# Performance work log

Measured on AMD Instinct MI355X. Metric: run time of the kernel, lower is better.

Reference implementation:

```python
import jax, jax.numpy as jnp
import numpy as np
import math

B, T, C, H, DFF = 4, 2048, 1024, 16, 4096
HD = C // H
EPS = 1e-5


def _layernorm(x, g, b):
    mu = jnp.mean(x, axis=-1, keepdims=True)
    var = jnp.var(x, axis=-1, keepdims=True)
    return (x - mu) * jax.lax.rsqrt(var + EPS) * g + b


def _new_gelu(x):
    # 0.5*x*(1+tanh(sqrt(2/pi)*(x+0.044715*x^3)))
    c = math.sqrt(2.0 / math.pi)
    return 0.5 * x * (1.0 + jnp.tanh(c * (x + 0.044715 * x ** 3)))


def setup_inputs() -> dict:
    key = jax.random.key(0)
    ks = jax.random.split(key, 12)
    s = lambda fan_in: 1.0 / math.sqrt(fan_in)
    return {
        "x": jax.random.normal(ks[0], (B, T, C), jnp.float32),
        "ln1_g": jnp.ones((C,), jnp.float32),
        "ln1_b": jnp.zeros((C,), jnp.float32),
        "w_qkv": jax.random.normal(ks[1], (C, 3 * C), jnp.float32) * s(C),
        "b_qkv": jnp.zeros((3 * C,), jnp.float32),
        "w_o": jax.random.normal(ks[2], (C, C), jnp.float32) * s(C),
        "b_o": jnp.zeros((C,), jnp.float32),
        "ln2_g": jnp.ones((C,), jnp.float32),
        "ln2_b": jnp.zeros((C,), jnp.float32),
        "w_fc": jax.random.normal(ks[3], (C, DFF), jnp.float32) * s(C),
        "b_fc": jnp.zeros((DFF,), jnp.float32),
        "w_proj": jax.random.normal(ks[4], (DFF, C), jnp.float32) * s(DFF),
        "b_proj": jnp.zeros((C,), jnp.float32),
    }


def reference(x, ln1_g, ln1_b, w_qkv, b_qkv, w_o, b_o, ln2_g, ln2_b, w_fc, b_fc, w_proj, b_proj):
    # --- attention sub-block ---
    h = _layernorm(x, ln1_g, ln1_b)
    qkv = h @ w_qkv + b_qkv                                  # (B,T,3C)
    q, k, v = jnp.split(qkv, 3, axis=-1)
    q = q.reshape(B, T, H, HD).transpose(0, 2, 1, 3)          # (B,H,T,hd)
    k = k.reshape(B, T, H, HD).transpose(0, 2, 1, 3)
    v = v.reshape(B, T, H, HD).transpose(0, 2, 1, 3)
    scores = jnp.einsum("bhqd,bhkd->bhqk", q, k) / math.sqrt(HD)
    causal = jnp.tril(jnp.ones((T, T), jnp.bool_))            # (T,T)
    scores = jnp.where(causal[None, None], scores, -jnp.inf)
    probs = jax.nn.softmax(scores, axis=-1)
    attn = jnp.einsum("bhqk,bhkd->bhqd", probs, v)
    attn = attn.transpose(0, 2, 1, 3).reshape(B, T, C)
    x = x + attn @ w_o + b_o
    # --- MLP sub-block ---
    h2 = _layernorm(x, ln2_g, ln2_b)
    x = x + _new_gelu(h2 @ w_fc + b_fc) @ w_proj + b_proj
    return x
```

## Files before the change

### kernel.cpp

```cpp
#include <hip/hip_runtime.h>
#include <hip/hip_bf16.h>

using bf16 = __hip_bfloat16;
typedef __attribute__((ext_vector_type(8))) short bf16x8;
typedef __attribute__((ext_vector_type(4))) float f32x4;
typedef __attribute__((ext_vector_type(16))) float f32x16;

#define LOG2E 1.4426950408889634f

__device__ inline short f2b(float f) {
  __hip_bfloat16 h = __float2bfloat16(f);
  return *reinterpret_cast<short*>(&h);
}
__device__ inline float b2f(short s) {
  unsigned int u = ((unsigned int)(unsigned short)s) << 16;
  float f;
  __builtin_memcpy(&f, &u, 4);
  return f;
}
__device__ inline unsigned pk2(float a, float b) {
  return (unsigned)(unsigned short)f2b(a) |
         ((unsigned)(unsigned short)f2b(b) << 16);
}

__global__ __launch_bounds__(256) void transpose_cast_kernel(
    const float* __restrict__ in, bf16* __restrict__ out, int K, int N) {
  __shared__ float tile[32][33];
  int tx = threadIdx.x & 31;
  int ty = threadIdx.x >> 5;
  int n0 = blockIdx.x * 32, k0 = blockIdx.y * 32;
#pragma unroll
  for (int i = 0; i < 4; i++)
    tile[ty + i * 8][tx] = in[(size_t)(k0 + ty + i * 8) * N + n0 + tx];
  __syncthreads();
#pragma unroll
  for (int i = 0; i < 4; i++)
    out[(size_t)(n0 + ty + i * 8) * K + k0 + tx] =
        __float2bfloat16(tile[tx][ty + i * 8]);
}

__global__ __launch_bounds__(256) void transpose_v_kernel(
    const bf16* __restrict__ qkv, bf16* __restrict__ vt) {
  __shared__ short tile[64][66];
  const int bh = blockIdx.y;
  const int b = bh >> 4, h = bh & 15;
  const int t0 = blockIdx.x * 64;
  const int tid = threadIdx.x;
  const int r = tid >> 3, c8 = (tid & 7) * 8;
#pragma unroll
  for (int p = 0; p < 2; p++) {
    int t = r + p * 32;
    bf16x8 v = *(const bf16x8*)&qkv[(size_t)(b * 2048 + t0 + t) * 3072 + 2048 +
                                    h * 64 + c8];
#pragma unroll
    for (int i = 0; i < 8; i++) tile[t][c8 + i] = v[i];
  }
  __syncthreads();
#pragma unroll
  for (int p = 0; p < 2; p++) {
    int d = r + p * 32;
    int tt = c8;
    bf16x8 o;
#pragma unroll
    for (int i = 0; i < 8; i++) o[i] = tile[tt + i][d];
    *(bf16x8*)&vt[(size_t)(bh * 64 + d) * 2048 + t0 + tt] = o;
  }
}

__global__ __launch_bounds__(256) void ln_kernel(
    const float* __restrict__ x, const float* __restrict__ g,
    const float* __restrict__ b, bf16* __restrict__ out) {
  int row = blockIdx.x;
  const float4 v = ((const float4*)(x + (size_t)row * 1024))[threadIdx.x];
  float s = v.x + v.y + v.z + v.w;
  float ss = v.x * v.x + v.y * v.y + v.z * v.z + v.w * v.w;
#pragma unroll
  for (int off = 1; off < 64; off <<= 1) {
    s += __shfl_xor(s, off);
    ss += __shfl_xor(ss, off);
  }
  __shared__ float red[2][4];
  int w = threadIdx.x >> 6, lane = threadIdx.x & 63;
  if (lane == 0) { red[0][w] = s; red[1][w] = ss; }
  __syncthreads();
  s = red[0][0] + red[0][1] + red[0][2] + red[0][3];
  ss = red[1][0] + red[1][1] + red[1][2] + red[1][3];
  float mu = s * (1.0f / 1024.0f);
  float var = ss * (1.0f / 1024.0f) - mu * mu;
  float rstd = rsqrtf(var + 1e-5f);
  const float4 gv = ((const float4*)g)[threadIdx.x];
  const float4 bv = ((const float4*)b)[threadIdx.x];
  short4 o4;
  o4.x = f2b((v.x - mu) * rstd * gv.x + bv.x);
  o4.y = f2b((v.y - mu) * rstd * gv.y + bv.y);
  o4.z = f2b((v.z - mu) * rstd * gv.z + bv.z);
  o4.w = f2b((v.w - mu) * rstd * gv.w + bv.w);
  ((short4*)out)[(size_t)row * 256 + threadIdx.x] = o4;
}

template <int EPI>
__global__ __launch_bounds__(256) void gemm_bt_kernel(
    const bf16* __restrict__ A, const bf16* __restrict__ Bt,
    const float* __restrict__ bias, const float* __restrict__ res,
    void* __restrict__ out, int M, int N, int K) {
  __shared__ short As[128 * 32];
  __shared__ short Bs[128 * 32];
  const int tid = threadIdx.x;
  const int w = tid >> 6, lane = tid & 63;
  const int wr = w >> 1, wc = w & 1;
  const int brow = blockIdx.y, bcol = blockIdx.x;

  f32x4 acc[4][4] = {};

  const int nk = K >> 5;
  for (int kt = 0; kt < nk; kt++) {
    __syncthreads();
#pragma unroll
    for (int j = 0; j < 2; j++) {
      int c = (j * 4 + w) * 64 + lane;
      int row = c >> 2, k8 = (c & 3) * 8;
      const bf16* ga = A + (size_t)(brow * 128 + row) * K + kt * 32 + k8;
      __builtin_amdgcn_global_load_lds(
          (const __attribute__((address_space(1))) unsigned int*)ga,
          (__attribute__((address_space(3))) unsigned int*)(As + (j * 4 + w) * 512),
          16, 0, 0);
      const bf16* gb = Bt + (size_t)(bcol * 128 + row) * K + kt * 32 + k8;
      __builtin_amdgcn_global_load_lds(
          (const __attribute__((address_space(1))) unsigned int*)gb,
          (__attribute__((address_space(3))) unsigned int*)(Bs + (j * 4 + w) * 512),
          16, 0, 0);
    }
    __syncthreads();
    bf16x8 af[4], bfr[4];
#pragma unroll
    for (int m = 0; m < 4; m++)
      af[m] = *(const bf16x8*)&As[(wr * 64 + m * 16 + (lane & 15)) * 32 +
                                  (lane >> 4) * 8];
#pragma unroll
    for (int n = 0; n < 4; n++)
      bfr[n] = *(const bf16x8*)&Bs[(wc * 64 + n * 16 + (lane & 15)) * 32 +
                                   (lane >> 4) * 8];
#pragma unroll
    for (int m = 0; m < 4; m++)
#pragma unroll
      for (int n = 0; n < 4; n++)
        acc[m][n] = __builtin_amdgcn_mfma_f32_16x16x32_bf16(af[m], bfr[n],
                                                            acc[m][n], 0, 0, 0);
  }

#pragma unroll
  for (int m = 0; m < 4; m++)
#pragma unroll
    for (int n = 0; n < 4; n++) {
      int gr0 = brow * 128 + wr * 64 + m * 16 + (lane >> 4) * 4;
      int gc = bcol * 128 + wc * 64 + n * 16 + (lane & 15);
      float bia = bias[gc];
#pragma unroll
      for (int j = 0; j < 4; j++) {
        float v = acc[m][n][j] + bia;
        size_t idx = (size_t)(gr0 + j) * N + gc;
        if constexpr (EPI == 0) {
          ((bf16*)out)[idx] = __float2bfloat16(v);
        } else if constexpr (EPI == 1) {
          ((float*)out)[idx] = v + res[idx];
        } else {
          float u = 0.7978845608028654f * (v + 0.044715f * v * v * v);
          float t = exp2f(u * (2.0f * LOG2E));
          float th = 1.0f - 2.0f / (t + 1.0f);
          ((bf16*)out)[idx] = __float2bfloat16(0.5f * v * (1.0f + th));
        }
      }
    }
}

__global__ __launch_bounds__(256) void attn_kernel(
    const bf16* __restrict__ qkv, const bf16* __restrict__ vt,
    bf16* __restrict__ attn) {
  const int bh = blockIdx.x;
  const int qt = blockIdx.y;
  const int b = bh >> 4, h = bh & 15;
  const int tid = threadIdx.x, w = tid >> 6, lane = tid & 63;
  const int col = lane & 31;
  const int hi = lane >> 5;

  __shared__ short Kl[64 * 64];
  __shared__ short Vl[64 * 64];

  const int qbase = qt * 128 + w * 32;
  const int qglob = qbase + col;
  const size_t qrow = (size_t)(b * 2048 + qglob);

  bf16x8 qf[4];
#pragma unroll
  for (int dks = 0; dks < 4; dks++) {
    bf16x8 raw =
        *(const bf16x8*)&qkv[qrow * 3072 + h * 64 + dks * 16 + hi * 8];
#pragma unroll
    for (int i = 0; i < 8; i++) qf[dks][i] = f2b(b2f(raw[i]) * 0.125f);
  }

  f32x16 ot[2] = {};
  float m = -1e30f, l = 0.0f;

  const int ktend = qt * 2 + 1;
  for (int kt = 0; kt <= ktend; kt++) {
    const int kv0 = kt * 64;
    __syncthreads();
#pragma unroll
    for (int j = 0; j < 2; j++) {
      int c = (j * 4 + w) * 64 + lane;
      int row = c >> 3;
      int sw8 = ((c & 7) ^ (row & 7)) * 8;
      const bf16* gk =
          qkv + (size_t)(b * 2048 + kv0 + row) * 3072 + 1024 + h * 64 + sw8;
      __builtin_amdgcn_global_load_lds(
          (const __attribute__((address_space(1))) unsigned int*)gk,
          (__attribute__((address_space(3))) unsigned int*)(Kl + (j * 4 + w) * 512),
          16, 0, 0);
      const bf16* gv = vt + (size_t)(bh * 64 + row) * 2048 + kv0 + sw8;
      __builtin_amdgcn_global_load_lds(
          (const __attribute__((address_space(1))) unsigned int*)gv,
          (__attribute__((address_space(3))) unsigned int*)(Vl + (j * 4 + w) * 512),
          16, 0, 0);
    }
    __syncthreads();

    if (kv0 <= qbase + 31) {
      f32x16 st[2] = {};
#pragma unroll
      for (int s = 0; s < 2; s++) {
        int kvrow = s * 32 + col;
        int swz = kvrow & 7;
#pragma unroll
        for (int dks = 0; dks < 4; dks++) {
          int ch = (dks * 2 + hi) ^ swz;
          bf16x8 kf = *(const bf16x8*)&Kl[kvrow * 64 + ch * 8];
          st[s] = __builtin_amdgcn_mfma_f32_32x32x16_bf16(kf, qf[dks], st[s],
                                                          0, 0, 0);
        }
      }
      if (kv0 + 63 > qbase) {
#pragma unroll
        for (int s = 0; s < 2; s++)
#pragma unroll
          for (int r = 0; r < 16; r++) {
            int kv = kv0 + s * 32 + (r & 3) + 8 * (r >> 2) + 4 * hi;
            if (kv > qglob) st[s][r] = -1e30f;
          }
      }
      float pmax = -1e30f;
#pragma unroll
      for (int s = 0; s < 2; s++)
#pragma unroll
        for (int r = 0; r < 16; r++) pmax = fmaxf(pmax, st[s][r]);
      pmax = fmaxf(pmax, __shfl_xor(pmax, 32));
      float mnew = fmaxf(m, pmax);
      float corr = exp2f((m - mnew) * LOG2E);
      m = mnew;
      float rs = 0.0f;
#pragma unroll
      for (int s = 0; s < 2; s++)
#pragma unroll
        for (int r = 0; r < 16; r++) {
          float pv = exp2f((st[s][r] - mnew) * LOG2E);
          st[s][r] = pv;
          rs += pv;
        }
      rs += __shfl_xor(rs, 32);
      l = l * corr + rs;
#pragma unroll
      for (int s = 0; s < 2; s++)
#pragma unroll
        for (int r = 0; r < 16; r++) ot[s][r] *= corr;

#pragma unroll
      for (int sub = 0; sub < 2; sub++) {
#pragma unroll
        for (int kl = 0; kl < 2; kl++) {
          unsigned A0 = pk2(st[sub][kl * 8 + 0], st[sub][kl * 8 + 1]);
          unsigned A1 = pk2(st[sub][kl * 8 + 2], st[sub][kl * 8 + 3]);
          unsigned B0 = pk2(st[sub][kl * 8 + 4], st[sub][kl * 8 + 5]);
          unsigned B1 = pk2(st[sub][kl * 8 + 6], st[sub][kl * 8 + 7]);
          unsigned sA0 = (unsigned)__shfl_xor((int)A0, 32);
          unsigned sA1 = (unsigned)__shfl_xor((int)A1, 32);
          unsigned sB0 = (unsigned)__shfl_xor((int)B0, 32);
          unsigned sB1 = (unsigned)__shfl_xor((int)B1, 32);
          union { unsigned u[4]; bf16x8 v; } pf;
          pf.u[0] = hi ? sB0 : A0;
          pf.u[1] = hi ? sB1 : A1;
          pf.u[2] = hi ? B0 : sA0;
          pf.u[3] = hi ? B1 : sA1;
          int ks = sub * 2 + kl;
#pragma unroll
          for (int ds = 0; ds < 2; ds++) {
            int drow = ds * 32 + col;
            int ch = (ks * 2 + hi) ^ (drow & 7);
            bf16x8 vf = *(const bf16x8*)&Vl[drow * 64 + ch * 8];
            ot[ds] = __builtin_amdgcn_mfma_f32_32x32x16_bf16(vf, pf.v, ot[ds],
                                                             0, 0, 0);
          }
        }
      }
    }
  }

  float rl = 1.0f / l;
#pragma unroll
  for (int ds = 0; ds < 2; ds++)
#pragma unroll
    for (int j = 0; j < 4; j++) {
      ushort4 o4;
      o4.x = (unsigned short)f2b(ot[ds][4 * j + 0] * rl);
      o4.y = (unsigned short)f2b(ot[ds][4 * j + 1] * rl);
      o4.z = (unsigned short)f2b(ot[ds][4 * j + 2] * rl);
      o4.w = (unsigned short)f2b(ot[ds][4 * j + 3] * rl);
      *(ushort4*)&attn[qrow * 1024 + h * 64 + 32 * ds + 8 * j + 4 * hi] = o4;
    }
}

extern "C" void kernel_launch(void* const* d_in, const int* in_sizes, int n_in,
                              void* d_out, int out_size, void* d_ws,
                              size_t ws_size, hipStream_t stream) {
  (void)in_sizes; (void)n_in; (void)out_size; (void)ws_size;
  const float* x      = (const float*)d_in[0];
  const float* ln1_g  = (const float*)d_in[1];
  const float* ln1_b  = (const float*)d_in[2];
  const float* w_qkv  = (const float*)d_in[3];
  const float* b_qkv  = (const float*)d_in[4];
  const float* w_o    = (const float*)d_in[5];
  const float* b_o    = (const float*)d_in[6];
  const float* ln2_g  = (const float*)d_in[7];
  const float* ln2_b  = (const float*)d_in[8];
  const float* w_fc   = (const float*)d_in[9];
  const float* b_fc   = (const float*)d_in[10];
  const float* w_proj = (const float*)d_in[11];
  const float* b_proj = (const float*)d_in[12];
  float* out = (float*)d_out;

  char* ws = (char*)d_ws;
  bf16* wt_qkv  = (bf16*)(ws + 0);
  bf16* wt_o    = (bf16*)(ws + 6291456);
  bf16* wt_fc   = (bf16*)(ws + 8388608);
  bf16* wt_proj = (bf16*)(ws + 16777216);
  float* x1     = (float*)(ws + 25165824);
  bf16* vtb     = (bf16*)(ws + 25165824);
  bf16* slotA   = (bf16*)(ws + 58720256);
  bf16* qkvb    = (bf16*)(ws + 75497472);
  bf16* gbuf    = (bf16*)(ws + 75497472);

  dim3 blk(256);
  transpose_cast_kernel<<<dim3(3072 / 32, 1024 / 32), blk, 0, stream>>>(
      w_qkv, wt_qkv, 1024, 3072);
  transpose_cast_kernel<<<dim3(1024 / 32, 1024 / 32), blk, 0, stream>>>(
      w_o, wt_o, 1024, 1024);
  transpose_cast_kernel<<<dim3(4096 / 32, 1024 / 32), blk, 0, stream>>>(
      w_fc, wt_fc, 1024, 4096);
  transpose_cast_kernel<<<dim3(1024 / 32, 4096 / 32), blk, 0, stream>>>(
      w_proj, wt_proj, 4096, 1024);

  ln_kernel<<<8192, blk, 0, stream>>>(x, ln1_g, ln1_b, slotA);
  gemm_bt_kernel<0><<<dim3(3072 / 128, 8192 / 128), blk, 0, stream>>>(
      slotA, wt_qkv, b_qkv, nullptr, qkvb, 8192, 3072, 1024);
  transpose_v_kernel<<<dim3(32, 64), blk, 0, stream>>>(qkvb, vtb);
  attn_kernel<<<dim3(64, 16), blk, 0, stream>>>(qkvb, vtb, slotA);
  gemm_bt_kernel<1><<<dim3(1024 / 128, 8192 / 128), blk, 0, stream>>>(
      slotA, wt_o, b_o, x, x1, 8192, 1024, 1024);
  ln_kernel<<<8192, blk, 0, stream>>>(x1, ln2_g, ln2_b, slotA);
  gemm_bt_kernel<2><<<dim3(4096 / 128, 8192 / 128), blk, 0, stream>>>(
      slotA, wt_fc, b_fc, nullptr, gbuf, 8192, 4096, 1024);
  gemm_bt_kernel<1><<<dim3(1024 / 128, 8192 / 128), blk, 0, stream>>>(
      gbuf, wt_proj, b_proj, x1, out, 8192, 1024, 4096);
}
```

Before: 471.3 us.

## Double-buffer attention K/V, add lazy softmax rescale, XCD-swizzle GEMM grid

The attention kernel now double-buffers K/V tiles in LDS, prefetching the next tile while computing the current one. It folds log2e into Q so the hardware v_exp_f32 can be used, and skips the running-max rescale unless the max grows by more than 8. It also processes query tiles in reverse order so the longest causal rows start first, and changes the LDS swizzle. The GEMMs use a 1D grid with a remapping intended to spread tiles across XCDs for better cache locality. Packed bf16 conversion instructions and a workspace re-layout are added; the lazy rescale and raw exp2 trade some numerical headroom for fewer instructions.

```diff
diff --git a/kernel.cpp b/kernel.cpp
--- a/kernel.cpp
+++ b/kernel.cpp
@@ -18,9 +18,15 @@
   __builtin_memcpy(&f, &u, 4);
   return f;
 }
-__device__ inline unsigned pk2(float a, float b) {
-  return (unsigned)(unsigned short)f2b(a) |
-         ((unsigned)(unsigned short)f2b(b) << 16);
+__device__ inline unsigned cvtpk(float a, float b) {
+  unsigned r;
+  asm("v_cvt_pk_bf16_f32 %0, %1, %2" : "=v"(r) : "v"(a), "v"(b));
+  return r;
+}
+__device__ inline float exp2_fast(float x) {
+  float r;
+  asm("v_exp_f32 %0, %1" : "=v"(r) : "v"(x));
+  return r;
 }
 
 __global__ __launch_bounds__(256) void transpose_cast_kernel(
@@ -90,16 +96,14 @@
   float rstd = rsqrtf(var + 1e-5f);
   const float4 gv = ((const float4*)g)[threadIdx.x];
   const float4 bv = ((const float4*)b)[threadIdx.x];
-  short4 o4;
-  o4.x = f2b((v.x - mu) * rstd * gv.x + bv.x);
-  o4.y = f2b((v.y - mu) * rstd * gv.y + bv.y);
-  o4.z = f2b((v.z - mu) * rstd * gv.z + bv.z);
-  o4.w = f2b((v.w - mu) * rstd * gv.w + bv.w);
-  ((short4*)out)[(size_t)row * 256 + threadIdx.x] = o4;
+  uint2 o2;
+  o2.x = cvtpk((v.x - mu) * rstd * gv.x + bv.x, (v.y - mu) * rstd * gv.y + bv.y);
+  o2.y = cvtpk((v.z - mu) * rstd * gv.z + bv.z, (v.w - mu) * rstd * gv.w + bv.w);
+  ((uint2*)out)[(size_t)row * 256 + threadIdx.x] = o2;
 }
 
 template <int EPI>
-__global__ __launch_bounds__(256) void gemm_bt_kernel(
+__global__ __launch_bounds__(256) void gemm128_kernel(
     const bf16* __restrict__ A, const bf16* __restrict__ Bt,
     const float* __restrict__ bias, const float* __restrict__ res,
     void* __restrict__ out, int M, int N, int K) {
@@ -108,7 +112,12 @@
   const int tid = threadIdx.x;
   const int w = tid >> 6, lane = tid & 63;
   const int wr = w >> 1, wc = w & 1;
-  const int brow = blockIdx.y, bcol = blockIdx.x;
+
+  const int nwg = gridDim.x;
+  const int gy = M >> 7;
+  const int flat = blockIdx.x;
+  const int sw = (flat & 7) * (nwg >> 3) + (flat >> 3);
+  const int bcol = sw / gy, brow = sw % gy;
 
   f32x4 acc[4][4] = {};
 
@@ -161,12 +170,12 @@
         size_t idx = (size_t)(gr0 + j) * N + gc;
         if constexpr (EPI == 0) {
           ((bf16*)out)[idx] = __float2bfloat16(v);
-        } else if constexpr (EPI == 1) {
+        } else if constexpr (EPI == 5) {
           ((float*)out)[idx] = v + res[idx];
         } else {
           float u = 0.7978845608028654f * (v + 0.044715f * v * v * v);
-          float t = exp2f(u * (2.0f * LOG2E));
-          float th = 1.0f - 2.0f / (t + 1.0f);
+          float t2 = exp2_fast(u * (2.0f * LOG2E));
+          float th = 1.0f - 2.0f / (t2 + 1.0f);
           ((bf16*)out)[idx] = __float2bfloat16(0.5f * v * (1.0f + th));
         }
       }
@@ -177,66 +186,82 @@
     const bf16* __restrict__ qkv, const bf16* __restrict__ vt,
     bf16* __restrict__ attn) {
   const int bh = blockIdx.x;
-  const int qt = blockIdx.y;
+  const int qt = 15 - blockIdx.y;
   const int b = bh >> 4, h = bh & 15;
   const int tid = threadIdx.x, w = tid >> 6, lane = tid & 63;
   const int col = lane & 31;
   const int hi = lane >> 5;
 
-  __shared__ short Kl[64 * 64];
-  __shared__ short Vl[64 * 64];
+  __shared__ short Kl[2][64 * 64];
+  __shared__ short Vl[2][64 * 64];
 
   const int qbase = qt * 128 + w * 32;
   const int qglob = qbase + col;
   const size_t qrow = (size_t)(b * 2048 + qglob);
 
-  bf16x8 qf[4];
+  union U8 { unsigned u[4]; bf16x8 v; };
+  U8 qf[4];
 #pragma unroll
   for (int dks = 0; dks < 4; dks++) {
     bf16x8 raw =
         *(const bf16x8*)&qkv[qrow * 3072 + h * 64 + dks * 16 + hi * 8];
 #pragma unroll
-    for (int i = 0; i < 8; i++) qf[dks][i] = f2b(b2f(raw[i]) * 0.125f);
-  }
-
-  f32x16 ot[2] = {};
-  float m = -1e30f, l = 0.0f;
-
-  const int ktend = qt * 2 + 1;
-  for (int kt = 0; kt <= ktend; kt++) {
-    const int kv0 = kt * 64;
-    __syncthreads();
+    for (int p = 0; p < 4; p++)
+      qf[dks].u[p] = cvtpk(b2f(raw[2 * p]) * (0.125f * LOG2E),
+                           b2f(raw[2 * p + 1]) * (0.125f * LOG2E));
+  }
+
+  auto stage = [&](int kt, int buf) {
+    const int kv0s = kt * 64;
 #pragma unroll
     for (int j = 0; j < 2; j++) {
       int c = (j * 4 + w) * 64 + lane;
       int row = c >> 3;
-      int sw8 = ((c & 7) ^ (row & 7)) * 8;
+      int sw8 = ((c & 7) ^ ((row >> 1) & 7)) * 8;
       const bf16* gk =
-          qkv + (size_t)(b * 2048 + kv0 + row) * 3072 + 1024 + h * 64 + sw8;
+          qkv + (size_t)(b * 2048 + kv0s + row) * 3072 + 1024 + h * 64 + sw8;
       __builtin_amdgcn_global_load_lds(
           (const __attribute__((address_space(1))) unsigned int*)gk,
-          (__attribute__((address_space(3))) unsigned int*)(Kl + (j * 4 + w) * 512),
+          (__attribute__((address_space(3))) unsigned int*)(
+              &Kl[buf][(j * 4 + w) * 512]),
           16, 0, 0);
-      const bf16* gv = vt + (size_t)(bh * 64 + row) * 2048 + kv0 + sw8;
+      const bf16* gv = vt + (size_t)(bh * 64 + row) * 2048 + kv0s + sw8;
       __builtin_amdgcn_global_load_lds(
           (const __attribute__((address_space(1))) unsigned int*)gv,
-          (__attribute__((address_space(3))) unsigned int*)(Vl + (j * 4 + w) * 512),
+          (__attribute__((address_space(3))) unsigned int*)(
+              &Vl[buf][(j * 4 + w) * 512]),
           16, 0, 0);
     }
-    __syncthreads();
+  };
+
+  f32x16 ot[2] = {};
+  float m = -1e30f, l = 0.0f;
+
+  const int ktend = qt * 2 + 1;
+  stage(0, 0);
+  for (int kt = 0; kt <= ktend; kt++) {
+    const int kv0 = kt * 64;
+    const int cur = kt & 1;
+    if (kt < ktend) {
+      stage(kt + 1, cur ^ 1);
+      asm volatile("s_waitcnt vmcnt(4)" ::: "memory");
+    } else {
+      asm volatile("s_waitcnt vmcnt(0)" ::: "memory");
+    }
+    __builtin_amdgcn_s_barrier();
 
     if (kv0 <= qbase + 31) {
       f32x16 st[2] = {};
 #pragma unroll
       for (int s = 0; s < 2; s++) {
         int kvrow = s * 32 + col;
-        int swz = kvrow & 7;
+        int swz = (kvrow >> 1) & 7;
 #pragma unroll
         for (int dks = 0; dks < 4; dks++) {
           int ch = (dks * 2 + hi) ^ swz;
-          bf16x8 kf = *(const bf16x8*)&Kl[kvrow * 64 + ch * 8];
-          st[s] = __builtin_amdgcn_mfma_f32_32x32x16_bf16(kf, qf[dks], st[s],
-                                                          0, 0, 0);
+          bf16x8 kf = *(const bf16x8*)&Kl[cur][kvrow * 64 + ch * 8];
+          st[s] = __builtin_amdgcn_mfma_f32_32x32x16_bf16(kf, qf[dks].v,
+                                                          st[s], 0, 0, 0);
         }
       }
       if (kv0 + 63 > qbase) {
@@ -248,44 +273,50 @@
             if (kv > qglob) st[s][r] = -1e30f;
           }
       }
-      float pmax = -1e30f;
+      float vm[16];
+#pragma unroll
+      for (int i = 0; i < 16; i++) vm[i] = fmaxf(st[0][i], st[1][i]);
+#pragma unroll
+      for (int w2 = 8; w2 >= 1; w2 >>= 1)
+#pragma unroll
+        for (int i = 0; i < w2; i++) vm[i] = fmaxf(vm[i], vm[i + w2]);
+      float pmax = fmaxf(vm[0], __shfl_xor(vm[0], 32));
+      if (!__all(pmax - m <= 8.0f)) {
+        float mnew = fmaxf(m, pmax);
+        float corr = exp2_fast(m - mnew);
+        m = mnew;
+        l *= corr;
+#pragma unroll
+        for (int s = 0; s < 2; s++)
+#pragma unroll
+          for (int r = 0; r < 16; r++) ot[s][r] *= corr;
+      }
 #pragma unroll
       for (int s = 0; s < 2; s++)
 #pragma unroll
-        for (int r = 0; r < 16; r++) pmax = fmaxf(pmax, st[s][r]);
-      pmax = fmaxf(pmax, __shfl_xor(pmax, 32));
-      float mnew = fmaxf(m, pmax);
-      float corr = exp2f((m - mnew) * LOG2E);
-      m = mnew;
-      float rs = 0.0f;
-#pragma unroll
-      for (int s = 0; s < 2; s++)
-#pragma unroll
-        for (int r = 0; r < 16; r++) {
-          float pv = exp2f((st[s][r] - mnew) * LOG2E);
-          st[s][r] = pv;
-          rs += pv;
-        }
-      rs += __shfl_xor(rs, 32);
-      l = l * corr + rs;
-#pragma unroll
-      for (int s = 0; s < 2; s++)
-#pragma unroll
-        for (int r = 0; r < 16; r++) ot[s][r] *= corr;
+        for (int r = 0; r < 16; r++) st[s][r] = exp2_fast(st[s][r] - m);
+      float vs[16];
+#pragma unroll
+      for (int i = 0; i < 16; i++) vs[i] = st[0][i] + st[1][i];
+#pragma unroll
+      for (int w2 = 8; w2 >= 1; w2 >>= 1)
+#pragma unroll
+        for (int i = 0; i < w2; i++) vs[i] += vs[i + w2];
+      l += vs[0] + __shfl_xor(vs[0], 32);
 
 #pragma unroll
       for (int sub = 0; sub < 2; sub++) {
 #pragma unroll
         for (int kl = 0; kl < 2; kl++) {
-          unsigned A0 = pk2(st[sub][kl * 8 + 0], st[sub][kl * 8 + 1]);
-          unsigned A1 = pk2(st[sub][kl * 8 + 2], st[sub][kl * 8 + 3]);
-          unsigned B0 = pk2(st[sub][kl * 8 + 4], st[sub][kl * 8 + 5]);
-          unsigned B1 = pk2(st[sub][kl * 8 + 6], st[sub][kl * 8 + 7]);
+          unsigned A0 = cvtpk(st[sub][kl * 8 + 0], st[sub][kl * 8 + 1]);
+          unsigned A1 = cvtpk(st[sub][kl * 8 + 2], st[sub][kl * 8 + 3]);
+          unsigned B0 = cvtpk(st[sub][kl * 8 + 4], st[sub][kl * 8 + 5]);
+          unsigned B1 = cvtpk(st[sub][kl * 8 + 6], st[sub][kl * 8 + 7]);
           unsigned sA0 = (unsigned)__shfl_xor((int)A0, 32);
           unsigned sA1 = (unsigned)__shfl_xor((int)A1, 32);
           unsigned sB0 = (unsigned)__shfl_xor((int)B0, 32);
           unsigned sB1 = (unsigned)__shfl_xor((int)B1, 32);
-          union { unsigned u[4]; bf16x8 v; } pf;
+          U8 pf;
           pf.u[0] = hi ? sB0 : A0;
           pf.u[1] = hi ? sB1 : A1;
           pf.u[2] = hi ? B0 : sA0;
@@ -294,14 +325,15 @@
 #pragma unroll
           for (int ds = 0; ds < 2; ds++) {
             int drow = ds * 32 + col;
-            int ch = (ks * 2 + hi) ^ (drow & 7);
-            bf16x8 vf = *(const bf16x8*)&Vl[drow * 64 + ch * 8];
+            int ch = (ks * 2 + hi) ^ ((drow >> 1) & 7);
+            bf16x8 vf = *(const bf16x8*)&Vl[cur][drow * 64 + ch * 8];
             ot[ds] = __builtin_amdgcn_mfma_f32_32x32x16_bf16(vf, pf.v, ot[ds],
                                                              0, 0, 0);
           }
         }
       }
     }
+    __builtin_amdgcn_s_barrier();
   }
 
   float rl = 1.0f / l;
@@ -309,12 +341,10 @@
   for (int ds = 0; ds < 2; ds++)
 #pragma unroll
     for (int j = 0; j < 4; j++) {
-      ushort4 o4;
-      o4.x = (unsigned short)f2b(ot[ds][4 * j + 0] * rl);
-      o4.y = (unsigned short)f2b(ot[ds][4 * j + 1] * rl);
-      o4.z = (unsigned short)f2b(ot[ds][4 * j + 2] * rl);
-      o4.w = (unsigned short)f2b(ot[ds][4 * j + 3] * rl);
-      *(ushort4*)&attn[qrow * 1024 + h * 64 + 32 * ds + 8 * j + 4 * hi] = o4;
+      uint2 o2;
+      o2.x = cvtpk(ot[ds][4 * j + 0] * rl, ot[ds][4 * j + 1] * rl);
+      o2.y = cvtpk(ot[ds][4 * j + 2] * rl, ot[ds][4 * j + 3] * rl);
+      *(uint2*)&attn[qrow * 1024 + h * 64 + 32 * ds + 8 * j + 4 * hi] = o2;
     }
 }
 
@@ -338,15 +368,16 @@
   float* out = (float*)d_out;
 
   char* ws = (char*)d_ws;
-  bf16* wt_qkv  = (bf16*)(ws + 0);
-  bf16* wt_o    = (bf16*)(ws + 6291456);
-  bf16* wt_fc   = (bf16*)(ws + 8388608);
-  bf16* wt_proj = (bf16*)(ws + 16777216);
-  float* x1     = (float*)(ws + 25165824);
-  bf16* vtb     = (bf16*)(ws + 25165824);
-  bf16* slotA   = (bf16*)(ws + 58720256);
-  bf16* qkvb    = (bf16*)(ws + 75497472);
-  bf16* gbuf    = (bf16*)(ws + 75497472);
+  const size_t MB = 1048576;
+  float* x1     = (float*)(ws + 0);
+  bf16* slotA   = (bf16*)(ws + 32 * MB);
+  bf16* wt_qkv  = (bf16*)(ws + 48 * MB);
+  bf16* wt_o    = (bf16*)(ws + 54 * MB);
+  bf16* wt_fc   = (bf16*)(ws + 56 * MB);
+  bf16* wt_proj = (bf16*)(ws + 64 * MB);
+  bf16* qkvb    = (bf16*)(ws + 72 * MB);
+  bf16* vtb     = (bf16*)(ws + 120 * MB);
+  bf16* gbuf    = (bf16*)(ws + 72 * MB);
 
   dim3 blk(256);
   transpose_cast_kernel<<<dim3(3072 / 32, 1024 / 32), blk, 0, stream>>>(
@@ -359,15 +390,15 @@
       w_proj, wt_proj, 4096, 1024);
 
   ln_kernel<<<8192, blk, 0, stream>>>(x, ln1_g, ln1_b, slotA);
-  gemm_bt_kernel<0><<<dim3(3072 / 128, 8192 / 128), blk, 0, stream>>>(
+  gemm128_kernel<0><<<dim3(1536), blk, 0, stream>>>(
       slotA, wt_qkv, b_qkv, nullptr, qkvb, 8192, 3072, 1024);
   transpose_v_kernel<<<dim3(32, 64), blk, 0, stream>>>(qkvb, vtb);
   attn_kernel<<<dim3(64, 16), blk, 0, stream>>>(qkvb, vtb, slotA);
-  gemm_bt_kernel<1><<<dim3(1024 / 128, 8192 / 128), blk, 0, stream>>>(
+  gemm128_kernel<5><<<dim3(512), blk, 0, stream>>>(
       slotA, wt_o, b_o, x, x1, 8192, 1024, 1024);
   ln_kernel<<<8192, blk, 0, stream>>>(x1, ln2_g, ln2_b, slotA);
-  gemm_bt_kernel<2><<<dim3(4096 / 128, 8192 / 128), blk, 0, stream>>>(
+  gemm128_kernel<2><<<dim3(2048), blk, 0, stream>>>(
       slotA, wt_fc, b_fc, nullptr, gbuf, 8192, 4096, 1024);
-  gemm_bt_kernel<1><<<dim3(1024 / 128, 8192 / 128), blk, 0, stream>>>(
+  gemm128_kernel<5><<<dim3(512), blk, 0, stream>>>(
       gbuf, wt_proj, b_proj, x1, out, 8192, 1024, 4096);
 }
```

After: 440.7 us. -6.5%, faster.
